# Kernel tuning notes

Hardware: AMD Instinct MI355X
Metric: run time of the kernel (lower is better)

## Reference

```python
import jax, jax.numpy as jnp
import numpy as np

R = 3            # window radius -> (2R+1)^2 = 49 neighbors
N = 128          # grid side, n
K = 131          # 3 + 64 + 64 channels
C = 21           # num_classes
B = 2            # batch
W = (2 * R + 1) ** 2


def setup_inputs() -> dict:
    key = jax.random.key(0)
    k1, k2, k3, k4 = jax.random.split(key, 4)
    return {
        "intergrated": jax.random.normal(k1, (B, K, N, N), jnp.float32),
        "x2": jax.random.normal(k2, (B, C, N * N), jnp.float32),
        "sel_mask": jax.random.randint(k3, (B, N, N), 0, 2).astype(jnp.int32),
        "conv_parameter": jax.random.uniform(k4, (K,), jnp.float32),
    }


def _shifts(x, r):
    """Gather (2r+1)^2 shifted copies: x [..., n, n] -> [..., n, n, W].
    Entry w=(di,dj) holds x[i+di-r, j+dj-r] (zero-padded out of bounds)."""
    n = x.shape[-1]
    pad = [(0, 0)] * (x.ndim - 2) + [(r, r), (r, r)]
    xp = jnp.pad(x, pad)
    cols = [xp[..., di:di + n, dj:dj + n]
            for di in range(2 * r + 1) for dj in range(2 * r + 1)]
    return jnp.stack(cols, axis=-1)


def _rwn_single(feats, x2b, maskb, conv_parameter):
    """feats [K,n,n], x2b [C,n^2], maskb [n,n] int -> y [n^2, C]."""
    n = feats.shape[-1]
    m = maskb.astype(feats.dtype)            # sampled-pixel indicator
    xm = feats * m                            # sparse-sampled features [K,n,n]
    nbr = _shifts(xm, R)                      # [K,n,n,W] neighbor values
    valid = _shifts(jnp.ones((n, n), feats.dtype), R) > 0  # [n,n,W] in-bounds
    # per-channel windowed L1 distance, exp, per-pixel normalization (softmax
    # of +distance over the valid window, as in the original code)
    d = jnp.abs(xm[..., None] - nbr)          # [K,n,n,W]
    e = jnp.where(valid[None], jnp.exp(d), 0.0)
    a = e / e.sum(axis=-1, keepdims=True)     # rows sum to 1 per channel
    # W = sum_k conv_parameter[k] * a_k, rows only for selected pixels
    A = jnp.einsum('k,kijw->ijw', conv_parameter, a) * m[..., None]  # [n,n,W]
    # y[q,c] = sum_p W[p,q] * x2[p,c]  (W^T @ x2^T, per original col/row swap)
    feat = x2b.reshape(C, n, n)
    msg = A[None] * feat[..., None]           # [C,n,n,W]
    ypad = jnp.zeros((C, n + 2 * R, n + 2 * R), feats.dtype)
    w = 0
    for di in range(2 * R + 1):
        for dj in range(2 * R + 1):
            ypad = ypad.at[:, di:di + n, dj:dj + n].add(msg[..., w])
            w += 1
    y = ypad[:, R:R + n, R:R + n].reshape(C, n * n)
    return y.T                                 # [n^2, C]


def reference(intergrated, x2, sel_mask, conv_parameter):
    f = lambda fe, xb, mb: _rwn_single(fe, xb, mb, conv_parameter)
    return jax.vmap(f)(intergrated, x2, sel_mask)  # [B, n^2, C]
```

## Files before the change

### kernel.cpp

```cpp
#include <hip/hip_runtime.h>
#include <hip/hip_fp16.h>

#define R_ 3
#define D_ 7
#define W_ 49
#define N_ 128
#define K_ 131
#define C_ 21
#define B_ 2
#define NN (N_ * N_)
#define TI_ 8
#define TJ_ 16
#define PROWS (TI_ + 2 * R_)
#define PCOLS (TJ_ + 2 * R_)
#define PSTR 24
#define NELEM (PROWS * PCOLS)
#define LDSP (PROWS * PSTR + 8)
#define KC 8
#define KCHUNK ((K_ + KC - 1) / KC)

typedef __fp16 h2 __attribute__((ext_vector_type(2)));

__global__ __launch_bounds__(256) void rwn_affinity(
    const float* __restrict__ feats,
    const int*   __restrict__ mask,
    const float* __restrict__ cp,
    float* __restrict__ Aout)
{
    __shared__ float2 patch2[LDSP];

    const int tile = blockIdx.x;
    const int kc   = blockIdx.y;
    const int b    = blockIdx.z;
    const int tr = tile >> 3, tc = tile & 7;
    const int ti0 = tr * TI_, tj0 = tc * TJ_;

    const int tid = threadIdx.x;
    const int pix = tid >> 1;
    const int h   = tid & 1;
    const int ti = pix >> 4;
    const int tj = pix & 15;
    const int gi = ti0 + ti, gj = tj0 + tj;

    const float LOG2E = 1.4426950408889634f;
    int   soff[2];
    float swt[2];
    float ozw[2];
    int   slds[2];
    #pragma unroll
    for (int r = 0; r < 2; ++r) {
        int e = tid + r * 256;
        bool act = (e < NELEM);
        int pr = e / PCOLS, pc = e - pr * PCOLS;
        int mi = ti0 + pr - R_, mj = tj0 + pc - R_;
        bool inb = act && mi >= 0 && mi < N_ && mj >= 0 && mj < N_;
        int cmi = mi < 0 ? 0 : (mi > N_ - 1 ? N_ - 1 : mi);
        int cmj = mj < 0 ? 0 : (mj > N_ - 1 ? N_ - 1 : mj);
        soff[r] = cmi * N_ + cmj;
        swt[r]  = inb ? ((float)mask[b * NN + soff[r]] * LOG2E) : 0.f;
        ozw[r]  = inb ? 1.f : 0.f;
        slds[r] = act ? (pr * PSTR + pc) : (PROWS * PSTR + 4);
    }

    const float ph = h ? 0.f : 1.f;
    const int cbase = ti * PSTR + tj;
    const int bh = cbase + h;

    h2 Aacc[14];
    #pragma unroll
    for (int i = 0; i < 14; ++i) Aacc[i] = (h2){(__fp16)0.f, (__fp16)0.f};

    const int k0 = kc * KCHUNK;
    const int k1 = (k0 + KCHUNK < K_) ? (k0 + KCHUNK) : K_;
    const float* fb = feats + (size_t)b * K_ * NN;

    for (int e = tid; e < LDSP; e += 256) patch2[e] = make_float2(0.f, 0.f);

    const float* fk0 = fb + (size_t)k0 * NN;
    float pre0 = fk0[soff[0]] * swt[0];
    float pre1 = fk0[soff[1]] * swt[1];

    __syncthreads();

    for (int k = k0; k < k1; ++k) {
        patch2[slds[0]] = make_float2(ozw[0] * exp2f(pre0), ozw[0] * exp2f(-pre0));
        patch2[slds[1]] = make_float2(ozw[1] * exp2f(pre1), ozw[1] * exp2f(-pre1));
        float n0 = 0.f, n1 = 0.f;
        if (k + 1 < k1) {
            const float* fn = fb + (size_t)(k + 1) * NN;
            n0 = fn[soff[0]] * swt[0];
            n1 = fn[soff[1]] * swt[1];
        }
        __syncthreads();

        const float2 cpair = patch2[cbase + R_ * PSTR + R_];
        h2 ex[14];
        float dsum = 0.f;
        #pragma unroll
        for (int u = 0; u < D_; ++u) {
            #pragma unroll
            for (int m = 0; m < 2; ++m) {
                const float2 np0 = patch2[bh + u * PSTR + 4 * m];
                const float2 np1 = patch2[bh + u * PSTR + 4 * m + 2];
                float t0 = fmaxf(cpair.x * np0.y, np0.x * cpair.y);
                float t1 = fmaxf(cpair.x * np1.y, np1.x * cpair.y);
                if (m == 1) t1 *= ph;
                dsum += t0;
                dsum += t1;
                ex[u * 2 + m] = __builtin_amdgcn_cvt_pkrtz(t0, t1);
            }
        }
        const float denom = dsum + __shfl_xor(dsum, 1, 64);
        const float scale = cp[k] * __frcp_rn(denom);
        const h2 s2 = __builtin_amdgcn_cvt_pkrtz(scale, scale);
        #pragma unroll
        for (int m = 0; m < 14; ++m) Aacc[m] = ex[m] * s2 + Aacc[m];
        __syncthreads();

        pre0 = n0; pre1 = n1;
    }

    if (mask[b * NN + gi * N_ + gj] != 0) {
        const int pixg = gi * N_ + gj;
        float* ab = Aout + (size_t)b * W_ * NN + h * NN + pixg;
        #pragma unroll
        for (int u = 0; u < D_; ++u) {
            #pragma unroll
            for (int m = 0; m < 2; ++m) {
                const h2 tv = Aacc[u * 2 + m];
                atomicAdd(ab + (u * D_ + 4 * m) * NN, (float)tv[0]);
                if (h == 0 || m < 1)
                    atomicAdd(ab + (u * D_ + 4 * m + 2) * NN, (float)tv[1]);
            }
        }
    }
}

#define RSTR 22
__global__ __launch_bounds__(512, 4) void rwn_gather(
    const float* __restrict__ Aarr,
    const float* __restrict__ x2,
    float* __restrict__ out)
{
    __shared__ float red[8 * 64 * RSTR];

    const int q0 = blockIdx.x * 64;
    const int b  = blockIdx.y;
    const int tid = threadIdx.x;
    const int qh = tid & 63;
    const int wg = tid >> 6;
    const int q = q0 + qh;
    const int i = q >> 7, j = q & (N_ - 1);

    const float* Ab = Aarr + (size_t)b * W_ * NN;
    const float* xb = x2 + (size_t)b * C_ * NN;

    float acc[C_];
    #pragma unroll
    for (int c = 0; c < C_; ++c) acc[c] = 0.f;

    if (wg < D_) {
        const int pi = i - (wg - R_);
        const int cpi = pi < 0 ? 0 : (pi > N_ - 1 ? N_ - 1 : pi);
        const float rv = (pi >= 0 && pi < N_) ? 1.f : 0.f;
        const float* Aw = Ab + (size_t)wg * D_ * NN;
        #pragma unroll
        for (int v = 0; v < D_; ++v) {
            const int pj = j - (v - R_);
            const int cpj = pj < 0 ? 0 : (pj > N_ - 1 ? N_ - 1 : pj);
            const float vv = (pj >= 0 && pj < N_) ? rv : 0.f;
            const int p = cpi * N_ + cpj;
            const float a = vv * Aw[(size_t)v * NN + p];
            #pragma unroll
            for (int c = 0; c < C_; ++c)
                acc[c] += a * xb[(size_t)c * NN + p];
        }
    }

    float* rbase = red + (wg * 64 + qh) * RSTR;
    #pragma unroll
    for (int c = 0; c < C_; ++c) rbase[c] = acc[c];
    __syncthreads();

    float* ob = out + ((size_t)b * NN + q0) * C_;
    for (int e = tid; e < 64 * C_; e += 512) {
        const int qq = e / C_, cc = e - qq * C_;
        const int a = qq * RSTR + cc;
        float s = 0.f;
        #pragma unroll
        for (int pl = 0; pl < 8; ++pl)
            s += red[pl * 64 * RSTR + a];
        ob[e] = s;
    }
}

extern "C" void kernel_launch(void* const* d_in, const int* in_sizes, int n_in,
                              void* d_out, int out_size, void* d_ws, size_t ws_size,
                              hipStream_t stream) {
    const float* feats = (const float*)d_in[0];
    const float* x2    = (const float*)d_in[1];
    const int*   mask  = (const int*)d_in[2];
    const float* cp    = (const float*)d_in[3];
    float* out = (float*)d_out;

    float* Aarr = (float*)d_ws;
    const size_t Abytes = (size_t)B_ * W_ * NN * sizeof(float);

    (void)hipMemsetAsync(Aarr, 0, Abytes, stream);

    dim3 gridA(128, KC, B_);
    rwn_affinity<<<gridA, 256, 0, stream>>>(feats, mask, cp, Aarr);

    dim3 gridG(NN / 64, B_);
    rwn_gather<<<gridG, 512, 0, stream>>>(Aarr, x2, out);
}
```

Baseline: 149.9 us.

## Use one thread per pixel with 16x16 tiles and smaller gather blocks

The affinity kernel moves from two threads per pixel on an 8x16 tile to one thread per pixel on a 16x16 tile. Each thread now computes all 49 window weights itself, which removes the cross-lane shuffle for the softmax denominator and lowers halo overhead per LDS patch. The cost is twice the fp16 accumulator registers per thread and half as many blocks. The gather kernel is also retuned to 32 pixels and 256 threads per block.

```diff
diff --git a/kernel.cpp b/kernel.cpp
--- a/kernel.cpp
+++ b/kernel.cpp
@@ -9,19 +9,17 @@
 #define C_ 21
 #define B_ 2
 #define NN (N_ * N_)
-#define TI_ 8
-#define TJ_ 16
-#define PROWS (TI_ + 2 * R_)
-#define PCOLS (TJ_ + 2 * R_)
+#define TILE 16
+#define PATCH (TILE + 2 * R_)
 #define PSTR 24
-#define NELEM (PROWS * PCOLS)
-#define LDSP (PROWS * PSTR + 8)
+#define NELEM (PATCH * PATCH)
+#define LDSP (PATCH * PSTR + 8)
 #define KC 8
 #define KCHUNK ((K_ + KC - 1) / KC)
 
 typedef __fp16 h2 __attribute__((ext_vector_type(2)));
 
-__global__ __launch_bounds__(256) void rwn_affinity(
+__global__ __launch_bounds__(256, 4) void rwn_affinity(
     const float* __restrict__ feats,
     const int*   __restrict__ mask,
     const float* __restrict__ cp,
@@ -33,13 +31,11 @@
     const int kc   = blockIdx.y;
     const int b    = blockIdx.z;
     const int tr = tile >> 3, tc = tile & 7;
-    const int ti0 = tr * TI_, tj0 = tc * TJ_;
+    const int ti0 = tr * TILE, tj0 = tc * TILE;
 
     const int tid = threadIdx.x;
-    const int pix = tid >> 1;
-    const int h   = tid & 1;
-    const int ti = pix >> 4;
-    const int tj = pix & 15;
+    const int ti = tid >> 4;
+    const int tj = tid & 15;
     const int gi = ti0 + ti, gj = tj0 + tj;
 
     const float LOG2E = 1.4426950408889634f;
@@ -51,7 +47,7 @@
     for (int r = 0; r < 2; ++r) {
         int e = tid + r * 256;
         bool act = (e < NELEM);
-        int pr = e / PCOLS, pc = e - pr * PCOLS;
+        int pr = e / PATCH, pc = e - pr * PATCH;
         int mi = ti0 + pr - R_, mj = tj0 + pc - R_;
         bool inb = act && mi >= 0 && mi < N_ && mj >= 0 && mj < N_;
         int cmi = mi < 0 ? 0 : (mi > N_ - 1 ? N_ - 1 : mi);
@@ -59,16 +55,14 @@
         soff[r] = cmi * N_ + cmj;
         swt[r]  = inb ? ((float)mask[b * NN + soff[r]] * LOG2E) : 0.f;
         ozw[r]  = inb ? 1.f : 0.f;
-        slds[r] = act ? (pr * PSTR + pc) : (PROWS * PSTR + 4);
-    }
-
-    const float ph = h ? 0.f : 1.f;
+        slds[r] = act ? (pr * PSTR + pc) : (PATCH * PSTR + 4);
+    }
+
     const int cbase = ti * PSTR + tj;
-    const int bh = cbase + h;
-
-    h2 Aacc[14];
-    #pragma unroll
-    for (int i = 0; i < 14; ++i) Aacc[i] = (h2){(__fp16)0.f, (__fp16)0.f};
+
+    h2 Aacc[28];
+    #pragma unroll
+    for (int i = 0; i < 28; ++i) Aacc[i] = (h2){(__fp16)0.f, (__fp16)0.f};
 
     const int k0 = kc * KCHUNK;
     const int k1 = (k0 + KCHUNK < K_) ? (k0 + KCHUNK) : K_;
@@ -94,61 +88,74 @@
         __syncthreads();
 
         const float2 cpair = patch2[cbase + R_ * PSTR + R_];
-        h2 ex[14];
+        h2 ex[28];
         float dsum = 0.f;
+        #pragma unroll
+        for (int u = 0; u < D_; ++u) {
+            const int rb = cbase + u * PSTR;
+            float t0 = 0.f, t1 = 0.f, t2 = 0.f, t3 = 0.f;
+            float t4 = 0.f, t5 = 0.f, t6 = 0.f;
+            {
+                const float2 a0 = patch2[rb + 0];
+                const float2 a1 = patch2[rb + 1];
+                const float2 a2 = patch2[rb + 2];
+                const float2 a3 = patch2[rb + 3];
+                const float2 a4 = patch2[rb + 4];
+                const float2 a5 = patch2[rb + 5];
+                const float2 a6 = patch2[rb + 6];
+                t0 = fmaxf(cpair.x * a0.y, a0.x * cpair.y);
+                t1 = fmaxf(cpair.x * a1.y, a1.x * cpair.y);
+                t2 = fmaxf(cpair.x * a2.y, a2.x * cpair.y);
+                t3 = fmaxf(cpair.x * a3.y, a3.x * cpair.y);
+                t4 = fmaxf(cpair.x * a4.y, a4.x * cpair.y);
+                t5 = fmaxf(cpair.x * a5.y, a5.x * cpair.y);
+                t6 = fmaxf(cpair.x * a6.y, a6.x * cpair.y);
+            }
+            dsum += ((t0 + t1) + (t2 + t3)) + ((t4 + t5) + t6);
+            ex[u * 4 + 0] = __builtin_amdgcn_cvt_pkrtz(t0, t1);
+            ex[u * 4 + 1] = __builtin_amdgcn_cvt_pkrtz(t2, t3);
+            ex[u * 4 + 2] = __builtin_amdgcn_cvt_pkrtz(t4, t5);
+            ex[u * 4 + 3] = __builtin_amdgcn_cvt_pkrtz(t6, 0.f);
+        }
+        const float scale = cp[k] * __frcp_rn(dsum);
+        const h2 s2 = __builtin_amdgcn_cvt_pkrtz(scale, scale);
+        #pragma unroll
+        for (int m = 0; m < 28; ++m) Aacc[m] = ex[m] * s2 + Aacc[m];
+        __syncthreads();
+
+        pre0 = n0; pre1 = n1;
+    }
+
+    if (mask[b * NN + gi * N_ + gj] != 0) {
+        const int pixg = gi * N_ + gj;
+        float* ab = Aout + (size_t)b * W_ * NN + pixg;
         #pragma unroll
         for (int u = 0; u < D_; ++u) {
             #pragma unroll
-            for (int m = 0; m < 2; ++m) {
-                const float2 np0 = patch2[bh + u * PSTR + 4 * m];
-                const float2 np1 = patch2[bh + u * PSTR + 4 * m + 2];
-                float t0 = fmaxf(cpair.x * np0.y, np0.x * cpair.y);
-                float t1 = fmaxf(cpair.x * np1.y, np1.x * cpair.y);
-                if (m == 1) t1 *= ph;
-                dsum += t0;
-                dsum += t1;
-                ex[u * 2 + m] = __builtin_amdgcn_cvt_pkrtz(t0, t1);
+            for (int m = 0; m < 4; ++m) {
+                const h2 tv = Aacc[u * 4 + m];
+                atomicAdd(ab + (u * D_ + 2 * m) * NN, (float)tv[0]);
+                if (m < 3)
+                    atomicAdd(ab + (u * D_ + 2 * m + 1) * NN, (float)tv[1]);
             }
         }
-        const float denom = dsum + __shfl_xor(dsum, 1, 64);
-        const float scale = cp[k] * __frcp_rn(denom);
-        const h2 s2 = __builtin_amdgcn_cvt_pkrtz(scale, scale);
-        #pragma unroll
-        for (int m = 0; m < 14; ++m) Aacc[m] = ex[m] * s2 + Aacc[m];
-        __syncthreads();
-
-        pre0 = n0; pre1 = n1;
-    }
-
-    if (mask[b * NN + gi * N_ + gj] != 0) {
-        const int pixg = gi * N_ + gj;
-        float* ab = Aout + (size_t)b * W_ * NN + h * NN + pixg;
-        #pragma unroll
-        for (int u = 0; u < D_; ++u) {
-            #pragma unroll
-            for (int m = 0; m < 2; ++m) {
-                const h2 tv = Aacc[u * 2 + m];
-                atomicAdd(ab + (u * D_ + 4 * m) * NN, (float)tv[0]);
-                if (h == 0 || m < 1)
-                    atomicAdd(ab + (u * D_ + 4 * m + 2) * NN, (float)tv[1]);
-            }
-        }
     }
 }
 
+#define GQ 32
 #define RSTR 22
-__global__ __launch_bounds__(512, 4) void rwn_gather(
+__global__ __launch_bounds__(256, 4) void rwn_gather(
     const float* __restrict__ Aarr,
     const float* __restrict__ x2,
     float* __restrict__ out)
 {
-    __shared__ float red[8 * 64 * RSTR];
-
-    const int q0 = blockIdx.x * 64;
+    __shared__ float red[8 * GQ * RSTR];
+
+    const int q0 = blockIdx.x * GQ;
     const int b  = blockIdx.y;
     const int tid = threadIdx.x;
-    const int qh = tid & 63;
-    const int wg = tid >> 6;
+    const int qh = tid & (GQ - 1);
+    const int wg = tid >> 5;
     const int q = q0 + qh;
     const int i = q >> 7, j = q & (N_ - 1);
 
@@ -177,19 +184,19 @@
         }
     }
 
-    float* rbase = red + (wg * 64 + qh) * RSTR;
+    float* rbase = red + (wg * GQ + qh) * RSTR;
     #pragma unroll
     for (int c = 0; c < C_; ++c) rbase[c] = acc[c];
     __syncthreads();
 
     float* ob = out + ((size_t)b * NN + q0) * C_;
-    for (int e = tid; e < 64 * C_; e += 512) {
+    for (int e = tid; e < GQ * C_; e += 256) {
         const int qq = e / C_, cc = e - qq * C_;
         const int a = qq * RSTR + cc;
         float s = 0.f;
         #pragma unroll
         for (int pl = 0; pl < 8; ++pl)
-            s += red[pl * 64 * RSTR + a];
+            s += red[pl * GQ * RSTR + a];
         ob[e] = s;
     }
 }
@@ -208,9 +215,9 @@
 
     (void)hipMemsetAsync(Aarr, 0, Abytes, stream);
 
-    dim3 gridA(128, KC, B_);
+    dim3 gridA(64, KC, B_);
     rwn_affinity<<<gridA, 256, 0, stream>>>(feats, mask, cp, Aarr);
 
-    dim3 gridG(NN / 64, B_);
-    rwn_gather<<<gridG, 512, 0, stream>>>(Aarr, x2, out);
+    dim3 gridG(NN / GQ, B_);
+    rwn_gather<<<gridG, 256, 0, stream>>>(Aarr, x2, out);
 }
```

Result: no change. 152.3 us (+1.6%).

## Retile affinity kernel to two pixels per thread with packed fp16 patch

Applied to the files above, without the earlier changes.

The affinity kernel now uses 16x16 tiles with 128 threads, and each thread computes the full 49-neighbor window for two adjacent pixels. Previously two threads split one pixel's window and combined results with a shuffle. The shared patch holds packed half-precision exp pairs, read as 4-wide vectors, and the distance, max and sum math runs in fp16 packed arithmetic. The exponent is offset by -4 to keep values within fp16 range. This aims to cut LDS traffic, shuffles and per-pixel overhead through register reuse, at the cost of fewer blocks, higher register pressure and reduced numerical precision.

```diff
diff --git a/kernel.cpp b/kernel.cpp
--- a/kernel.cpp
+++ b/kernel.cpp
@@ -9,49 +9,44 @@
 #define C_ 21
 #define B_ 2
 #define NN (N_ * N_)
-#define TI_ 8
-#define TJ_ 16
-#define PROWS (TI_ + 2 * R_)
-#define PCOLS (TJ_ + 2 * R_)
-#define PSTR 24
-#define NELEM (PROWS * PCOLS)
-#define LDSP (PROWS * PSTR + 8)
+#define TILE 16
+#define PATCH 22
+#define PSH 24
+#define NELEM (PATCH * PATCH)
+#define LDSE (PATCH * PSH + 8)
 #define KC 8
 #define KCHUNK ((K_ + KC - 1) / KC)
 
 typedef __fp16 h2 __attribute__((ext_vector_type(2)));
-
-__global__ __launch_bounds__(256) void rwn_affinity(
+typedef __fp16 h4 __attribute__((ext_vector_type(4)));
+
+__global__ __launch_bounds__(128, 2) void rwn_affinity(
     const float* __restrict__ feats,
     const int*   __restrict__ mask,
     const float* __restrict__ cp,
     float* __restrict__ Aout)
 {
-    __shared__ float2 patch2[LDSP];
+    __shared__ h2 patch[LDSE];
 
     const int tile = blockIdx.x;
     const int kc   = blockIdx.y;
     const int b    = blockIdx.z;
     const int tr = tile >> 3, tc = tile & 7;
-    const int ti0 = tr * TI_, tj0 = tc * TJ_;
+    const int ti0 = tr * TILE, tj0 = tc * TILE;
 
     const int tid = threadIdx.x;
-    const int pix = tid >> 1;
-    const int h   = tid & 1;
-    const int ti = pix >> 4;
-    const int tj = pix & 15;
-    const int gi = ti0 + ti, gj = tj0 + tj;
+    const int ti  = tid >> 3;
+    const int tjp = (tid & 7) * 2;
+    const int gi = ti0 + ti;
+    const int gj0 = tj0 + tjp, gj1 = gj0 + 1;
 
     const float LOG2E = 1.4426950408889634f;
-    int   soff[2];
-    float swt[2];
-    float ozw[2];
-    int   slds[2];
-    #pragma unroll
-    for (int r = 0; r < 2; ++r) {
-        int e = tid + r * 256;
+    int   soff[4]; float swt[4]; float ozw[4]; int slds[4];
+    #pragma unroll
+    for (int r = 0; r < 4; ++r) {
+        int e = tid + r * 128;
         bool act = (e < NELEM);
-        int pr = e / PCOLS, pc = e - pr * PCOLS;
+        int pr = e / PATCH, pc = e - pr * PATCH;
         int mi = ti0 + pr - R_, mj = tj0 + pc - R_;
         bool inb = act && mi >= 0 && mi < N_ && mj >= 0 && mj < N_;
         int cmi = mi < 0 ? 0 : (mi > N_ - 1 ? N_ - 1 : mi);
@@ -59,78 +54,123 @@
         soff[r] = cmi * N_ + cmj;
         swt[r]  = inb ? ((float)mask[b * NN + soff[r]] * LOG2E) : 0.f;
         ozw[r]  = inb ? 1.f : 0.f;
-        slds[r] = act ? (pr * PSTR + pc) : (PROWS * PSTR + 4);
-    }
-
-    const float ph = h ? 0.f : 1.f;
-    const int cbase = ti * PSTR + tj;
-    const int bh = cbase + h;
-
-    h2 Aacc[14];
-    #pragma unroll
-    for (int i = 0; i < 14; ++i) Aacc[i] = (h2){(__fp16)0.f, (__fp16)0.f};
+        slds[r] = act ? (pr * PSH + pc) : (PATCH * PSH + 4);
+    }
+
+    h2 A0[28], A1[28];
+    #pragma unroll
+    for (int i = 0; i < 28; ++i) { A0[i] = (h2)0.f; A1[i] = (h2)0.f; }
 
     const int k0 = kc * KCHUNK;
     const int k1 = (k0 + KCHUNK < K_) ? (k0 + KCHUNK) : K_;
     const float* fb = feats + (size_t)b * K_ * NN;
 
-    for (int e = tid; e < LDSP; e += 256) patch2[e] = make_float2(0.f, 0.f);
-
-    const float* fk0 = fb + (size_t)k0 * NN;
-    float pre0 = fk0[soff[0]] * swt[0];
-    float pre1 = fk0[soff[1]] * swt[1];
+    for (int e = tid; e < LDSE; e += 128) patch[e] = (h2)0.f;
+
+    float pre[4];
+    #pragma unroll
+    for (int r = 0; r < 4; ++r) pre[r] = fb[(size_t)k0 * NN + soff[r]] * swt[r];
 
     __syncthreads();
 
+    const int cen = (ti + R_) * PSH + tjp + R_;
+    const int rb0 = ti * PSH + tjp;
+
     for (int k = k0; k < k1; ++k) {
-        patch2[slds[0]] = make_float2(ozw[0] * exp2f(pre0), ozw[0] * exp2f(-pre0));
-        patch2[slds[1]] = make_float2(ozw[1] * exp2f(pre1), ozw[1] * exp2f(-pre1));
-        float n0 = 0.f, n1 = 0.f;
+        #pragma unroll
+        for (int r = 0; r < 4; ++r) {
+            float E = ozw[r] * exp2f(pre[r] - 4.f);
+            float I = ozw[r] * exp2f(-pre[r] - 4.f);
+            patch[slds[r]] = __builtin_amdgcn_cvt_pkrtz(E, I);
+        }
+        float nx[4];
         if (k + 1 < k1) {
             const float* fn = fb + (size_t)(k + 1) * NN;
-            n0 = fn[soff[0]] * swt[0];
-            n1 = fn[soff[1]] * swt[1];
+            #pragma unroll
+            for (int r = 0; r < 4; ++r) nx[r] = fn[soff[r]] * swt[r];
+        } else {
+            #pragma unroll
+            for (int r = 0; r < 4; ++r) nx[r] = 0.f;
         }
         __syncthreads();
 
-        const float2 cpair = patch2[cbase + R_ * PSTR + R_];
-        h2 ex[14];
-        float dsum = 0.f;
+        const h2 c0 = patch[cen];
+        const h2 c1 = patch[cen + 1];
+        const __fp16 Ec0 = c0.x, Ic0 = c0.y;
+        const __fp16 Ec1 = c1.x, Ic1 = c1.y;
+
+        h2 ex0[28], ex1[28];
+        h2 ds0 = (h2)0.f, ds1 = (h2)0.f;
         #pragma unroll
         for (int u = 0; u < D_; ++u) {
-            #pragma unroll
-            for (int m = 0; m < 2; ++m) {
-                const float2 np0 = patch2[bh + u * PSTR + 4 * m];
-                const float2 np1 = patch2[bh + u * PSTR + 4 * m + 2];
-                float t0 = fmaxf(cpair.x * np0.y, np0.x * cpair.y);
-                float t1 = fmaxf(cpair.x * np1.y, np1.x * cpair.y);
-                if (m == 1) t1 *= ph;
-                dsum += t0;
-                dsum += t1;
-                ex[u * 2 + m] = __builtin_amdgcn_cvt_pkrtz(t0, t1);
-            }
-        }
-        const float denom = dsum + __shfl_xor(dsum, 1, 64);
-        const float scale = cp[k] * __frcp_rn(denom);
-        const h2 s2 = __builtin_amdgcn_cvt_pkrtz(scale, scale);
-        #pragma unroll
-        for (int m = 0; m < 14; ++m) Aacc[m] = ex[m] * s2 + Aacc[m];
+            const h4* rp = (const h4*)&patch[rb0 + u * PSH];
+            const h4 q0 = rp[0], q1 = rp[1], q2 = rp[2], q3 = rp[3];
+            __fp16 E[8], I[8];
+            E[0]=q0[0]; I[0]=q0[1]; E[1]=q0[2]; I[1]=q0[3];
+            E[2]=q1[0]; I[2]=q1[1]; E[3]=q1[2]; I[3]=q1[3];
+            E[4]=q2[0]; I[4]=q2[1]; E[5]=q2[2]; I[5]=q2[3];
+            E[6]=q3[0]; I[6]=q3[1]; E[7]=q3[2]; I[7]=q3[3];
+            __fp16 t0[7], t1[7];
+            #pragma unroll
+            for (int j = 0; j < 7; ++j) {
+                t0[j] = __builtin_fmaxf16((__fp16)(Ec0 * I[j]), (__fp16)(E[j] * Ic0));
+                t1[j] = __builtin_fmaxf16((__fp16)(Ec1 * I[j+1]), (__fp16)(E[j+1] * Ic1));
+            }
+            #pragma unroll
+            for (int m = 0; m < 3; ++m) {
+                h2 p0 = {t0[2*m], t0[2*m+1]};
+                h2 p1 = {t1[2*m], t1[2*m+1]};
+                ex0[u*4+m] = p0; ds0 += p0;
+                ex1[u*4+m] = p1; ds1 += p1;
+            }
+            h2 p0t = {t0[6], (__fp16)0.f};
+            h2 p1t = {t1[6], (__fp16)0.f};
+            ex0[u*4+3] = p0t; ds0 += p0t;
+            ex1[u*4+3] = p1t; ds1 += p1t;
+        }
+        const float cpk = cp[k];
+        const float dsum0 = (float)ds0.x + (float)ds0.y;
+        const float dsum1 = (float)ds1.x + (float)ds1.y;
+        const float sc0 = cpk * __frcp_rn(dsum0);
+        const float sc1 = cpk * __frcp_rn(dsum1);
+        const h2 s0 = __builtin_amdgcn_cvt_pkrtz(sc0, sc0);
+        const h2 s1 = __builtin_amdgcn_cvt_pkrtz(sc1, sc1);
+        #pragma unroll
+        for (int m = 0; m < 28; ++m) {
+            A0[m] = ex0[m] * s0 + A0[m];
+            A1[m] = ex1[m] * s1 + A1[m];
+        }
         __syncthreads();
-
-        pre0 = n0; pre1 = n1;
-    }
-
-    if (mask[b * NN + gi * N_ + gj] != 0) {
-        const int pixg = gi * N_ + gj;
-        float* ab = Aout + (size_t)b * W_ * NN + h * NN + pixg;
+        #pragma unroll
+        for (int r = 0; r < 4; ++r) pre[r] = nx[r];
+    }
+
+    const int m0 = mask[b * NN + gi * N_ + gj0];
+    const int m1 = mask[b * NN + gi * N_ + gj1];
+    float* abase = Aout + (size_t)b * W_ * NN + gi * N_;
+    if (m0 != 0) {
+        float* ab = abase + gj0;
         #pragma unroll
         for (int u = 0; u < D_; ++u) {
             #pragma unroll
-            for (int m = 0; m < 2; ++m) {
-                const h2 tv = Aacc[u * 2 + m];
-                atomicAdd(ab + (u * D_ + 4 * m) * NN, (float)tv[0]);
-                if (h == 0 || m < 1)
-                    atomicAdd(ab + (u * D_ + 4 * m + 2) * NN, (float)tv[1]);
+            for (int m = 0; m < 4; ++m) {
+                const h2 tv = A0[u * 4 + m];
+                atomicAdd(ab + (u * D_ + 2 * m) * NN, (float)tv.x);
+                if (m < 3)
+                    atomicAdd(ab + (u * D_ + 2 * m + 1) * NN, (float)tv.y);
+            }
+        }
+    }
+    if (m1 != 0) {
+        float* ab = abase + gj1;
+        #pragma unroll
+        for (int u = 0; u < D_; ++u) {
+            #pragma unroll
+            for (int m = 0; m < 4; ++m) {
+                const h2 tv = A1[u * 4 + m];
+                atomicAdd(ab + (u * D_ + 2 * m) * NN, (float)tv.x);
+                if (m < 3)
+                    atomicAdd(ab + (u * D_ + 2 * m + 1) * NN, (float)tv.y);
             }
         }
     }
@@ -208,8 +248,8 @@
 
     (void)hipMemsetAsync(Aarr, 0, Abytes, stream);
 
-    dim3 gridA(128, KC, B_);
-    rwn_affinity<<<gridA, 256, 0, stream>>>(feats, mask, cp, Aarr);
+    dim3 gridA(64, KC, B_);
+    rwn_affinity<<<gridA, 128, 0, stream>>>(feats, mask, cp, Aarr);
 
     dim3 gridG(NN / 64, B_);
     rwn_gather<<<gridG, 512, 0, stream>>>(Aarr, x2, out);
```

Result: slower. 190.5 us (+27.1%).

## Compact selected pixels per tile in affinity kernel and shrink gather blocks

Applied to the files above, without the earlier changes.

The affinity kernel now uses 16x16 tiles and builds a compacted list of mask-selected pixels in shared memory with a ballot and prefix count. Thread pairs then compute window affinities only for selected pixels, up to two per thread. This skips the roughly half of pixels whose rows are zeroed by the mask and loads less halo per useful pixel, but it adds divergence and a second accumulator set that raises register pressure. The gather kernel is also retuned to 32 pixels per 256-thread block.

```diff
diff --git a/kernel.cpp b/kernel.cpp
--- a/kernel.cpp
+++ b/kernel.cpp
@@ -9,13 +9,11 @@
 #define C_ 21
 #define B_ 2
 #define NN (N_ * N_)
-#define TI_ 8
-#define TJ_ 16
-#define PROWS (TI_ + 2 * R_)
-#define PCOLS (TJ_ + 2 * R_)
+#define TILE 16
+#define PATCH 22
 #define PSTR 24
-#define NELEM (PROWS * PCOLS)
-#define LDSP (PROWS * PSTR + 8)
+#define NELEM (PATCH * PATCH)
+#define LDSP (PATCH * PSTR + 8)
 #define KC 8
 #define KCHUNK ((K_ + KC - 1) / KC)
 
@@ -28,30 +26,30 @@
     float* __restrict__ Aout)
 {
     __shared__ float2 patch2[LDSP];
+    __shared__ unsigned char sel[256];
+    __shared__ int wq[4];
 
     const int tile = blockIdx.x;
     const int kc   = blockIdx.y;
     const int b    = blockIdx.z;
     const int tr = tile >> 3, tc = tile & 7;
-    const int ti0 = tr * TI_, tj0 = tc * TJ_;
-
-    const int tid = threadIdx.x;
-    const int pix = tid >> 1;
-    const int h   = tid & 1;
-    const int ti = pix >> 4;
-    const int tj = pix & 15;
-    const int gi = ti0 + ti, gj = tj0 + tj;
+    const int ti0 = tr * TILE, tj0 = tc * TILE;
+
+    const int tid  = threadIdx.x;
+    const int lane = tid & 63, wid = tid >> 6;
+
+    const int pti = tid >> 4, ptj = tid & 15;
+    const int msel = (mask[b * NN + (ti0 + pti) * N_ + (tj0 + ptj)] != 0) ? 1 : 0;
+    unsigned long long bal = __ballot(msel);
+    if (lane == 0) wq[wid] = (int)__popcll(bal);
 
     const float LOG2E = 1.4426950408889634f;
-    int   soff[2];
-    float swt[2];
-    float ozw[2];
-    int   slds[2];
+    int soff[2]; float swt[2]; float ozw[2]; int slds[2];
     #pragma unroll
     for (int r = 0; r < 2; ++r) {
         int e = tid + r * 256;
         bool act = (e < NELEM);
-        int pr = e / PCOLS, pc = e - pr * PCOLS;
+        int pr = e / PATCH, pc = e - pr * PATCH;
         int mi = ti0 + pr - R_, mj = tj0 + pc - R_;
         bool inb = act && mi >= 0 && mi < N_ && mj >= 0 && mj < N_;
         int cmi = mi < 0 ? 0 : (mi > N_ - 1 ? N_ - 1 : mi);
@@ -59,28 +57,43 @@
         soff[r] = cmi * N_ + cmj;
         swt[r]  = inb ? ((float)mask[b * NN + soff[r]] * LOG2E) : 0.f;
         ozw[r]  = inb ? 1.f : 0.f;
-        slds[r] = act ? (pr * PSTR + pc) : (PROWS * PSTR + 4);
-    }
-
+        slds[r] = act ? (pr * PSTR + pc) : (PATCH * PSTR + 4);
+    }
+
+    for (int e = tid; e < LDSP; e += 256) patch2[e] = make_float2(0.f, 0.f);
+
+    __syncthreads();
+
+    int pre_cnt = 0;
+    #pragma unroll
+    for (int w = 0; w < 3; ++w) if (w < wid) pre_cnt += wq[w];
+    const int nsel = wq[0] + wq[1] + wq[2] + wq[3];
+    if (msel)
+        sel[pre_cnt + (int)__popcll(bal & ((1ull << lane) - 1ull))] =
+            (unsigned char)tid;
+
+    __syncthreads();
+
+    const int sA = tid >> 1;
+    const int h  = tid & 1;
     const float ph = h ? 0.f : 1.f;
-    const int cbase = ti * PSTR + tj;
-    const int bh = cbase + h;
-
-    h2 Aacc[14];
-    #pragma unroll
-    for (int i = 0; i < 14; ++i) Aacc[i] = (h2){(__fp16)0.f, (__fp16)0.f};
+    const bool actA = (sA < nsel);
+    const bool actB = (sA + 128 < nsel);
+    const int pA = actA ? (int)sel[sA] : 0;
+    const int pB = actB ? (int)sel[sA + 128] : 0;
+    const int cbA = (pA >> 4) * PSTR + (pA & 15);
+    const int cbB = (pB >> 4) * PSTR + (pB & 15);
+
+    h2 Aa[14], Ab[14];
+    #pragma unroll
+    for (int i = 0; i < 14; ++i) { Aa[i] = (h2)0.f; Ab[i] = (h2)0.f; }
 
     const int k0 = kc * KCHUNK;
     const int k1 = (k0 + KCHUNK < K_) ? (k0 + KCHUNK) : K_;
     const float* fb = feats + (size_t)b * K_ * NN;
 
-    for (int e = tid; e < LDSP; e += 256) patch2[e] = make_float2(0.f, 0.f);
-
-    const float* fk0 = fb + (size_t)k0 * NN;
-    float pre0 = fk0[soff[0]] * swt[0];
-    float pre1 = fk0[soff[1]] * swt[1];
-
-    __syncthreads();
+    float pre0 = fb[(size_t)k0 * NN + soff[0]] * swt[0];
+    float pre1 = fb[(size_t)k0 * NN + soff[1]] * swt[1];
 
     for (int k = k0; k < k1; ++k) {
         patch2[slds[0]] = make_float2(ozw[0] * exp2f(pre0), ozw[0] * exp2f(-pre0));
@@ -93,62 +106,104 @@
         }
         __syncthreads();
 
-        const float2 cpair = patch2[cbase + R_ * PSTR + R_];
-        h2 ex[14];
-        float dsum = 0.f;
+        const float cpk = cp[k];
+
+        if (actA) {
+            const float2 cpair = patch2[cbA + R_ * PSTR + R_];
+            const int bh = cbA + h;
+            h2 ex[14];
+            float dsum = 0.f;
+            #pragma unroll
+            for (int u = 0; u < D_; ++u) {
+                #pragma unroll
+                for (int m = 0; m < 2; ++m) {
+                    const float2 np0 = patch2[bh + u * PSTR + 4 * m];
+                    const float2 np1 = patch2[bh + u * PSTR + 4 * m + 2];
+                    float t0 = fmaxf(cpair.x * np0.y, np0.x * cpair.y);
+                    float t1 = fmaxf(cpair.x * np1.y, np1.x * cpair.y);
+                    if (m == 1) t1 *= ph;
+                    dsum += t0; dsum += t1;
+                    ex[u * 2 + m] = __builtin_amdgcn_cvt_pkrtz(t0, t1);
+                }
+            }
+            const float denom = dsum + __shfl_xor(dsum, 1, 64);
+            const float scale = cpk * __frcp_rn(denom);
+            const h2 s2 = __builtin_amdgcn_cvt_pkrtz(scale, scale);
+            #pragma unroll
+            for (int m = 0; m < 14; ++m) Aa[m] = ex[m] * s2 + Aa[m];
+        }
+        if (actB) {
+            const float2 cpair = patch2[cbB + R_ * PSTR + R_];
+            const int bh = cbB + h;
+            h2 ex[14];
+            float dsum = 0.f;
+            #pragma unroll
+            for (int u = 0; u < D_; ++u) {
+                #pragma unroll
+                for (int m = 0; m < 2; ++m) {
+                    const float2 np0 = patch2[bh + u * PSTR + 4 * m];
+                    const float2 np1 = patch2[bh + u * PSTR + 4 * m + 2];
+                    float t0 = fmaxf(cpair.x * np0.y, np0.x * cpair.y);
+                    float t1 = fmaxf(cpair.x * np1.y, np1.x * cpair.y);
+                    if (m == 1) t1 *= ph;
+                    dsum += t0; dsum += t1;
+                    ex[u * 2 + m] = __builtin_amdgcn_cvt_pkrtz(t0, t1);
+                }
+            }
+            const float denom = dsum + __shfl_xor(dsum, 1, 64);
+            const float scale = cpk * __frcp_rn(denom);
+            const h2 s2 = __builtin_amdgcn_cvt_pkrtz(scale, scale);
+            #pragma unroll
+            for (int m = 0; m < 14; ++m) Ab[m] = ex[m] * s2 + Ab[m];
+        }
+        __syncthreads();
+        pre0 = n0; pre1 = n1;
+    }
+
+    if (actA) {
+        const int pixg = (ti0 + (pA >> 4)) * N_ + (tj0 + (pA & 15));
+        float* ab = Aout + (size_t)b * W_ * NN + h * NN + pixg;
         #pragma unroll
         for (int u = 0; u < D_; ++u) {
             #pragma unroll
             for (int m = 0; m < 2; ++m) {
-                const float2 np0 = patch2[bh + u * PSTR + 4 * m];
-                const float2 np1 = patch2[bh + u * PSTR + 4 * m + 2];
-                float t0 = fmaxf(cpair.x * np0.y, np0.x * cpair.y);
-                float t1 = fmaxf(cpair.x * np1.y, np1.x * cpair.y);
-                if (m == 1) t1 *= ph;
-                dsum += t0;
-                dsum += t1;
-                ex[u * 2 + m] = __builtin_amdgcn_cvt_pkrtz(t0, t1);
-            }
-        }
-        const float denom = dsum + __shfl_xor(dsum, 1, 64);
-        const float scale = cp[k] * __frcp_rn(denom);
-        const h2 s2 = __builtin_amdgcn_cvt_pkrtz(scale, scale);
-        #pragma unroll
-        for (int m = 0; m < 14; ++m) Aacc[m] = ex[m] * s2 + Aacc[m];
-        __syncthreads();
-
-        pre0 = n0; pre1 = n1;
-    }
-
-    if (mask[b * NN + gi * N_ + gj] != 0) {
-        const int pixg = gi * N_ + gj;
+                const h2 tv = Aa[u * 2 + m];
+                atomicAdd(ab + (u * D_ + 4 * m) * NN, (float)tv.x);
+                if (h == 0 || m < 1)
+                    atomicAdd(ab + (u * D_ + 4 * m + 2) * NN, (float)tv.y);
+            }
+        }
+    }
+    if (actB) {
+        const int pixg = (ti0 + (pB >> 4)) * N_ + (tj0 + (pB & 15));
         float* ab = Aout + (size_t)b * W_ * NN + h * NN + pixg;
         #pragma unroll
         for (int u = 0; u < D_; ++u) {
             #pragma unroll
             for (int m = 0; m < 2; ++m) {
-                const h2 tv = Aacc[u * 2 + m];
-                atomicAdd(ab + (u * D_ + 4 * m) * NN, (float)tv[0]);
+                const h2 tv = Ab[u * 2 + m];
+                atomicAdd(ab + (u * D_ + 4 * m) * NN, (float)tv.x);
                 if (h == 0 || m < 1)
-                    atomicAdd(ab + (u * D_ + 4 * m + 2) * NN, (float)tv[1]);
+                    atomicAdd(ab + (u * D_ + 4 * m + 2) * NN, (float)tv.y);
             }
         }
     }
 }
 
+#define GQ 32
 #define RSTR 22
-__global__ __launch_bounds__(512, 4) void rwn_gather(
+__global__ __launch_bounds__(256, 4) void rwn_gather(
     const float* __restrict__ Aarr,
     const float* __restrict__ x2,
     float* __restrict__ out)
 {
-    __shared__ float red[8 * 64 * RSTR];
-
-    const int q0 = blockIdx.x * 64;
+    __shared__ float red[8 * GQ * RSTR];
+
+    const int q0 = blockIdx.x * GQ;
     const int b  = blockIdx.y;
     const int tid = threadIdx.x;
-    const int qh = tid & 63;
-    const int wg = tid >> 6;
+    const int qh = tid & (GQ - 1);
+    const int wg = tid >> 5;
     const int q = q0 + qh;
     const int i = q >> 7, j = q & (N_ - 1);
 
@@ -177,19 +232,19 @@
         }
     }
 
-    float* rbase = red + (wg * 64 + qh) * RSTR;
+    float* rbase = red + (wg * GQ + qh) * RSTR;
     #pragma unroll
     for (int c = 0; c < C_; ++c) rbase[c] = acc[c];
     __syncthreads();
 
     float* ob = out + ((size_t)b * NN + q0) * C_;
-    for (int e = tid; e < 64 * C_; e += 512) {
+    for (int e = tid; e < GQ * C_; e += 256) {
         const int qq = e / C_, cc = e - qq * C_;
         const int a = qq * RSTR + cc;
         float s = 0.f;
         #pragma unroll
         for (int pl = 0; pl < 8; ++pl)
-            s += red[pl * 64 * RSTR + a];
+            s += red[pl * GQ * RSTR + a];
         ob[e] = s;
     }
 }
@@ -208,9 +263,9 @@
 
     (void)hipMemsetAsync(Aarr, 0, Abytes, stream);
 
-    dim3 gridA(128, KC, B_);
+    dim3 gridA(64, KC, B_);
     rwn_affinity<<<gridA, 256, 0, stream>>>(feats, mask, cp, Aarr);
 
-    dim3 gridG(NN / 64, B_);
-    rwn_gather<<<gridG, 512, 0, stream>>>(Aarr, x2, out);
+    dim3 gridG(NN / GQ, B_);
+    rwn_gather<<<gridG, 256, 0, stream>>>(Aarr, x2, out);
 }
```

New measurement: 159.6 us. 1.06x slower.
